# Optimization experiments

Measured on AMD Instinct MI355X. Metric: run time of the kernel, lower is better.

## Reference

```python
import jax, jax.numpy as jnp
import numpy as np

K, PS, WS, WT, NHEADS, STRIDE0_A, STRIDE0 = 7, 7, 8, 1, 1, 8, 4
SCALE = STRIDE0_A // STRIDE0  # index-upsampling factor (coarse stride 8 -> fine stride 4)


def _reflect(i, L):
    # dnls-style reflect bounds: i<0 -> -i, i>=L -> 2*(L-1)-i (single reflection suffices here)
    i = jnp.abs(i)
    return jnp.where(i >= L, 2 * (L - 1) - i, i)


def _patch_offsets(ps):
    pr = jnp.arange(ps) - ps // 2
    return jnp.stack(jnp.meshgrid(pr, pr, indexing='ij'), -1).reshape(-1, 2)  # [ps*ps, 2]


def _exact_search(vid0, vid1):
    # coarse windowed patch-product k-NN search (prod_with_heads), stride0_a query grid
    B, T, C, H, W = vid0.shape
    HD, Ch = NHEADS, C // NHEADS
    v0 = jnp.moveaxis(vid0, 2, -1)  # [B,T,H,W,C]
    v1 = jnp.moveaxis(vid1, 2, -1)
    nH, nW = H // STRIDE0_A, W // STRIDE0_A
    qt, qi, qj = [a.reshape(-1) for a in jnp.meshgrid(jnp.arange(T), jnp.arange(nH), jnp.arange(nW), indexing='ij')]
    qh, qw = qi * STRIDE0_A, qj * STRIDE0_A
    Q = qt.shape[0]
    st = 2 * WT + 1  # temporal window, shifted to stay in [0,T)
    t0 = jnp.clip(qt - WT, 0, T - st)
    offs = jnp.arange(WS) - WS // 2  # spatial window offsets, stride1=1
    ct = jnp.broadcast_to((t0[:, None] + jnp.arange(st))[:, :, None, None], (Q, st, WS, WS)).reshape(Q, -1)
    ch = jnp.broadcast_to((qh[:, None] + offs)[:, None, :, None], (Q, st, WS, WS)).reshape(Q, -1)
    cw = jnp.broadcast_to((qw[:, None] + offs)[:, None, None, :], (Q, st, WS, WS)).reshape(Q, -1)
    S = st * WS * WS
    poffs = _patch_offsets(PS)

    def body(acc, off):  # accumulate patch inner products one patch-pixel at a time (memory-light)
        dr, dc = off[0], off[1]
        p0 = v0[:, qt, _reflect(qh + dr, H), _reflect(qw + dc, W)]   # [B,Q,C]
        p1 = v1[:, ct, _reflect(ch + dr, H), _reflect(cw + dc, W)]   # [B,Q,S,C]
        d = jnp.einsum('bqnc,bqsnc->bnqs', p0.reshape(B, Q, HD, Ch), p1.reshape(B, Q, S, HD, Ch))
        return acc + d, None

    dists, _ = jax.lax.scan(jax.checkpoint(body), jnp.zeros((B, HD, Q, S), v0.dtype), poffs)
    vals, idx = jax.lax.top_k(dists, K)  # product search -> largest first
    qsel = jnp.arange(Q)[None, None, :, None]
    inds = jnp.stack([ct[qsel, idx], ch[qsel, idx], cw[qsel, idx]], -1)  # [B,HD,Q,K,3]
    return vals, inds


def _upsample_inds(inds_a, T, H, W):
    # interpolate_inds: replicate coarse inds to the fine stride0 grid, shifted by the
    # fine-query offset relative to its parent coarse query; anchor self at slot 0.
    nH, nW = H // STRIDE0_A, W // STRIDE0_A
    nHf, nWf = H // STRIDE0, W // STRIDE0
    ft, fi, fj = [a.reshape(-1) for a in jnp.meshgrid(jnp.arange(T), jnp.arange(nHf), jnp.arange(nWf), indexing='ij')]
    fh, fw = fi * STRIDE0, fj * STRIDE0
    ci = jnp.clip(fi // SCALE, 0, nH - 1)
    cj = jnp.clip(fj // SCALE, 0, nW - 1)
    qlin = ft * nH * nW + ci * nW + cj
    base = inds_a[:, :, qlin]  # [B,HD,Qf,K,3]
    dh = (fh - ci * STRIDE0_A)[None, None, :, None]
    dw = (fw - cj * STRIDE0_A)[None, None, :, None]
    it = base[..., 0]
    ih = _reflect(base[..., 1] + dh, H)
    iw = _reflect(base[..., 2] + dw, W)
    it = it.at[..., 0].set(ft[None, None, :])  # anchor_self=True
    ih = ih.at[..., 0].set(fh[None, None, :])
    iw = iw.at[..., 0].set(fw[None, None, :])
    return (ft, fh, fw), (it, ih, iw)


def _refine_dists(vid0, vid1, fq, cand):
    # prod_refine with ws_r=1: evaluate the patch product exactly at the given inds
    B, T, C, H, W = vid0.shape
    HD, Ch = NHEADS, C // NHEADS
    ft, fh, fw = fq
    it, ih, iw = cand
    Qf, k = it.shape[2], it.shape[3]
    v0 = jnp.moveaxis(vid0, 2, -1)                                # [B,T,H,W,C]
    v1h = jnp.moveaxis(vid1, 2, -1).reshape(B, T, H, W, HD, Ch)
    bidx = jnp.arange(B)[:, None, None, None]
    hidx = jnp.arange(HD)[None, :, None, None]
    poffs = _patch_offsets(PS)

    def body(acc, off):
        dr, dc = off[0], off[1]
        p0 = v0[:, ft, _reflect(fh + dr, H), _reflect(fw + dc, W)]              # [B,Qf,C]
        p1 = v1h[bidx, it, _reflect(ih + dr, H), _reflect(iw + dc, W), hidx]    # [B,HD,Qf,k,Ch]
        d = jnp.einsum('bqnc,bnqkc->bnqk', p0.reshape(B, Qf, HD, Ch), p1)
        return acc + d, None

    dists, _ = jax.lax.scan(jax.checkpoint(body), jnp.zeros((B, HD, Qf, k), v0.dtype), poffs)
    return dists


def setup_inputs() -> dict:
    key = jax.random.key(0)
    k0, k1 = jax.random.split(key)
    B, T, C, H, W = 1, 3, 64, 192, 192
    vid0 = jax.random.normal(k0, (B, T, C, H, W), dtype=jnp.float32)
    vid1 = jax.random.normal(k1, (B, T, C, H, W), dtype=jnp.float32)
    flows = jnp.zeros((B, T, 2, H, W), dtype=jnp.float32)  # accepted but unused (fflow/bflow=None)
    return {"vid0": vid0, "vid1": vid1, "flows": flows}


def reference(vid0, vid1, flows):
    B, T, C, H, W = vid0.shape
    dists_a, inds_a = _exact_search(vid0, vid1)            # coarse stride0_a search
    fq, cand = _upsample_inds(inds_a, T, H, W)             # interpolate inds to stride0 grid
    dists_f = _refine_dists(vid0, vid1, fq, cand)          # refine (fill) dists at fine inds
    inds_f = jnp.stack(cand, -1)                           # [B,HD,Qf,K,3]
    return dists_f, inds_f
```

## Files before the change

kernel.cpp:

```cpp
#include <hip/hip_runtime.h>
#include <math.h>

#define TT   3
#define CC   64
#define HH   192
#define WW   192
#define HWW  (HH*WW)
#define NHC  24
#define NWC  24
#define QC   1728
#define SC   192
#define NPIX 49
#define KK   7
#define NHF  48
#define NWF  48
#define QF   6912

__device__ __forceinline__ int reflect(int i, int L) {
  i = i < 0 ? -i : i;
  return (i >= L) ? (2 * (L - 1) - i) : i;
}

__global__ void transpose_tchw_thwc(const float* __restrict__ in0,
                                    const float* __restrict__ in1,
                                    float* __restrict__ out0,
                                    float* __restrict__ out1) {
  const float* in = blockIdx.y ? in1 : in0;
  float* out = blockIdx.y ? out1 : out0;
  int b = blockIdx.x;
  int x0 = (b % 3) * 64;
  int ty = b / 3;
  int t = ty / HH, y = ty % HH;

  __shared__ float tile[64][65];
  int lx = threadIdx.x & 63;
  int lc = threadIdx.x >> 6;

  const float* src = in + (size_t)t * CC * HWW + (size_t)y * WW + x0;
#pragma unroll
  for (int i = 0; i < 16; ++i) {
    int c = lc + i * 4;
    tile[c][lx] = src[(size_t)c * HWW + lx];
  }
  __syncthreads();
  float* dst = out + ((size_t)(t * HH + y) * WW + x0) * CC;
#pragma unroll
  for (int i = 0; i < 16; ++i) {
    int x = lc + i * 4;
    dst[(size_t)x * CC + lx] = tile[lx][x];
  }
}

__global__ __launch_bounds__(256, 3) void coarse_fma_kernel(
    const float* __restrict__ v0, const float* __restrict__ v1,
    float* __restrict__ dists) {
  int bid = blockIdx.x;
  int q = (bid & 7) * (QC / 8) + (bid >> 3);
  int qt = q / (NHC * NWC);
  int r = q % (NHC * NWC);
  int qh = (r / NWC) * 8;
  int qw = (r % NWC) * 8;

  __shared__ float4 region4[8 * 196];
  __shared__ float4 qbuf4[16 * 49];
  __shared__ float  wbuf[64 * 49];

  int tid = threadIdx.x;
  int s = tid & 63;
  int w = tid >> 6;
  int oi = s >> 3, oj = s & 7;

  int pxb[13];
#pragma unroll
  for (int i = 0; i < 13; ++i) {
    int p = w + 4 * i;
    if (p > 48) p = 48;
    pxb[i] = ((oi + p / 7) * 14 + (oj + p % 7)) * 16;
  }

  {
    const float* b0 = v0 + (size_t)qt * HWW * CC;
    for (int idx = tid; idx < 896; idx += 256) {
      int p = (idx & 7) | ((idx >> 7) << 3);
      int c4 = (idx >> 3) & 15;
      if (p < 49) {
        int ry = reflect(qh + p / 7 - 3, HH);
        int rx = reflect(qw + p % 7 - 3, WW);
        qbuf4[c4 * 49 + p] = *reinterpret_cast<const float4*>(
            b0 + ((size_t)ry * WW + rx) * CC + c4 * 4);
      }
    }
  }

  for (int ct = 0; ct < 3; ++ct) {
    const float* b1 = v1 + (size_t)ct * HWW * CC;
    float acc[13];
#pragma unroll
    for (int i = 0; i < 13; ++i) acc[i] = 0.f;

#pragma unroll
    for (int h = 0; h < 2; ++h) {
      __syncthreads();
      for (int idx = tid; idx < 1600; idx += 256) {
        int px = (idx & 7) | ((idx >> 6) << 3);
        int c4h = (idx >> 3) & 7;
        if (px < 196) {
          int ry = reflect(qh - 7 + px / 14, HH);
          int rx = reflect(qw - 7 + px % 14, WW);
          region4[c4h * 196 + px] = *reinterpret_cast<const float4*>(
              b1 + ((size_t)ry * WW + rx) * CC + (h * 8 + c4h) * 4);
        }
      }
      __syncthreads();

#pragma unroll
      for (int i = 0; i < 13; ++i) {
        if (i < 12 || w == 0) {
          int p = w + 4 * i;
          const char* rbase = reinterpret_cast<const char*>(region4) + pxb[i];
#pragma unroll
          for (int c4h = 0; c4h < 8; ++c4h) {
            float4 a = qbuf4[(h * 8 + c4h) * 49 + p];
            float4 b = *reinterpret_cast<const float4*>(rbase + c4h * 3136);
            acc[i] = fmaf(a.x, b.x, acc[i]);
            acc[i] = fmaf(a.y, b.y, acc[i]);
            acc[i] = fmaf(a.z, b.z, acc[i]);
            acc[i] = fmaf(a.w, b.w, acc[i]);
          }
        }
      }
    }

#pragma unroll
    for (int i = 0; i < 13; ++i) {
      if (i < 12 || w == 0) wbuf[s * 49 + (w + 4 * i)] = acc[i];
    }
    __syncthreads();
    if (tid < 64) {
      float a = 0.f;
      const float* wr = wbuf + tid * 49;
      for (int p = 0; p < NPIX; ++p)
        a = __fadd_rn(a, wr[p]);
      dists[(size_t)q * SC + ct * 64 + tid] = a;
    }
  }
}

__global__ __launch_bounds__(256) void topk_kernel(
    const float* __restrict__ dists, int* __restrict__ topk) {
  int q = blockIdx.x * 4 + (threadIdx.x >> 6);
  if (q >= QC) return;
  int lane = threadIdx.x & 63;
  const float* d = dists + (size_t)q * SC;
  float v[3] = {d[lane], d[lane + 64], d[lane + 128]};
  int tk = 0;
#pragma unroll
  for (int k = 0; k < KK; ++k) {
    float bv = -INFINITY;
    int bi = 0x7fffffff;
#pragma unroll
    for (int j = 0; j < 3; ++j) {
      if (!((tk >> j) & 1) && v[j] > bv) { bv = v[j]; bi = lane + j * 64; }
    }
#pragma unroll
    for (int off = 32; off > 0; off >>= 1) {
      float ov = __shfl_xor(bv, off, 64);
      int oi = __shfl_xor(bi, off, 64);
      if (ov > bv || (ov == bv && oi < bi)) { bv = ov; bi = oi; }
    }
    if ((bi & 63) == lane) tk |= 1 << (bi >> 6);
    if (lane == 0) topk[q * KK + k] = bi;
  }
}

__global__ __launch_bounds__(448, 7) void refine_kernel(
    const float* __restrict__ v0, const float* __restrict__ v1,
    const int* __restrict__ topk, float* __restrict__ out) {
  int bid = blockIdx.x;
  int f = (bid & 7) * (QF / 8) + (bid >> 3);
  int ft = f / (NHF * NWF);
  int r = f % (NHF * NWF);
  int fi = r / NWF, fj = r % NWF;
  int fh = fi * 4, fw = fj * 4;
  int ci = fi >> 1, cj = fj >> 1;
  int dh = (fi & 1) * 4, dw = (fj & 1) * 4;
  int qlin = ft * (NHC * NWC) + ci * NWC + cj;

  int tid = threadIdx.x;
  int lane = tid & 63;
  int k = tid >> 6;

  __shared__ float qs[NPIX * CC];

  {
    const float* b0 = v0 + (size_t)ft * HWW * CC;
#pragma unroll
    for (int i = 0; i < 7; ++i) {
      int idx = tid + i * 448;
      int p = idx >> 6, c = idx & 63;
      int ry = reflect(fh + p / 7 - 3, HH);
      int rx = reflect(fw + p % 7 - 3, WW);
      qs[idx] = b0[((size_t)ry * WW + rx) * CC + c];
    }
  }
  __syncthreads();

  int it, ih, iw;
  if (k == 0) {
    it = ft; ih = fh; iw = fw;
  } else {
    int s = topk[qlin * KK + k];
    int ti = s >> 6;
    int oi = (s >> 3) & 7, oj = s & 7;
    it = ti;
    ih = reflect(ci * 8 + oi - 4 + dh, HH);
    iw = reflect(cj * 8 + oj - 4 + dw, WW);
  }

  const float* b1 = v1 + (size_t)it * HWW * CC;
  float acc = 0.f;
#pragma unroll
  for (int pr = 0; pr < 7; ++pr) {
    int ry = reflect(ih + pr - 3, HH);
    const float* rowp = b1 + (size_t)ry * WW * CC + lane;
    float vals[7];
#pragma unroll
    for (int pc = 0; pc < 7; ++pc) {
      int rx = reflect(iw + pc - 3, WW);
      vals[pc] = rowp[(size_t)rx * CC];
    }
#pragma unroll
    for (int pc = 0; pc < 7; ++pc)
      acc = fmaf(qs[(pr * 7 + pc) * CC + lane], vals[pc], acc);
  }
#pragma unroll
  for (int off = 32; off > 0; off >>= 1)
    acc += __shfl_xor(acc, off, 64);
  if (lane == 0) {
    float* dout = out;
    float* iout = out + (size_t)QF * KK;
    dout[(size_t)f * KK + k] = acc;
    float* ip = iout + ((size_t)f * KK + k) * 3;
    ip[0] = (float)it;
    ip[1] = (float)ih;
    ip[2] = (float)iw;
  }
}

extern "C" void kernel_launch(void* const* d_in, const int* in_sizes, int n_in,
                              void* d_out, int out_size, void* d_ws,
                              size_t ws_size, hipStream_t stream) {
  const float* vid0 = (const float*)d_in[0];
  const float* vid1 = (const float*)d_in[1];
  float* out = (float*)d_out;

  char* ws = (char*)d_ws;
  float* dists = (float*)ws;
  size_t off = (size_t)QC * SC * sizeof(float);
  int* topk = (int*)(ws + off);
  off += (size_t)QC * KK * sizeof(int);
  off = (off + 255) & ~(size_t)255;
  float* v0t = (float*)(ws + off);
  size_t vbytes = (size_t)TT * HWW * CC * sizeof(float);
  float* v1t = (float*)(ws + off + vbytes);

  transpose_tchw_thwc<<<dim3(TT * HH * (WW / 64), 2), 256, 0, stream>>>(
      vid0, vid1, v0t, v1t);
  coarse_fma_kernel<<<QC, 256, 0, stream>>>(v0t, v1t, dists);
  topk_kernel<<<(QC * 64 + 255) / 256, 256, 0, stream>>>(dists, topk);
  refine_kernel<<<QF, 448, 0, stream>>>(v0t, v1t, topk, out);
}
```

Baseline: 288.0 us.

## Prefetch coarse region into registers and register-block two search offsets per thread

```diff
diff --git a/kernel.cpp b/kernel.cpp
--- a/kernel.cpp
+++ b/kernel.cpp
@@ -51,7 +51,7 @@
   }
 }
 
-__global__ __launch_bounds__(256, 3) void coarse_fma_kernel(
+__global__ __launch_bounds__(256, 4) void coarse_fma_kernel(
     const float* __restrict__ v0, const float* __restrict__ v1,
     float* __restrict__ dists) {
   int bid = blockIdx.x;
@@ -63,19 +63,39 @@
 
   __shared__ float4 region4[8 * 196];
   __shared__ float4 qbuf4[16 * 49];
-  __shared__ float  wbuf[64 * 49];
+  float* wbuf = (float*)region4;
 
   int tid = threadIdx.x;
-  int s = tid & 63;
+  int lane = tid & 63;
   int w = tid >> 6;
-  int oi = s >> 3, oj = s & 7;
-
-  int pxb[13];
-#pragma unroll
-  for (int i = 0; i < 13; ++i) {
-    int p = w + 4 * i;
+  int ph = lane >> 5;
+  int sA = lane & 31;
+  int oiA = sA >> 3, oj = sA & 7;
+  int rres = w + 4 * ph;
+
+  int pxb[7];
+#pragma unroll
+  for (int i = 0; i < 7; ++i) {
+    int p = rres + 8 * i;
     if (p > 48) p = 48;
-    pxb[i] = ((oi + p / 7) * 14 + (oj + p % 7)) * 16;
+    pxb[i] = ((oiA + p / 7) * 14 + (oj + p % 7)) * 16;
+  }
+
+  int srow[7], sdst[7];
+#pragma unroll
+  for (int j = 0; j < 7; ++j) {
+    int idx = tid + 256 * j;
+    int px = (idx & 7) | ((idx >> 6) << 3);
+    int c4h = (idx >> 3) & 7;
+    if (idx < 1600 && px < 196) {
+      int ry = reflect(qh - 7 + px / 14, HH);
+      int rx = reflect(qw - 7 + px % 14, WW);
+      srow[j] = (ry * WW + rx) * CC + c4h * 4;
+      sdst[j] = c4h * 196 + px;
+    } else {
+      srow[j] = 0;
+      sdst[j] = -1;
+    }
   }
 
   {
@@ -92,48 +112,70 @@
     }
   }
 
+  float4 rbuf[7];
+#pragma unroll
+  for (int j = 0; j < 7; ++j)
+    if (sdst[j] >= 0)
+      rbuf[j] = *reinterpret_cast<const float4*>(v1 + srow[j]);
+
   for (int ct = 0; ct < 3; ++ct) {
-    const float* b1 = v1 + (size_t)ct * HWW * CC;
-    float acc[13];
-#pragma unroll
-    for (int i = 0; i < 13; ++i) acc[i] = 0.f;
+    float accA[7], accB[7];
+#pragma unroll
+    for (int i = 0; i < 7; ++i) { accA[i] = 0.f; accB[i] = 0.f; }
 
 #pragma unroll
     for (int h = 0; h < 2; ++h) {
       __syncthreads();
-      for (int idx = tid; idx < 1600; idx += 256) {
-        int px = (idx & 7) | ((idx >> 6) << 3);
-        int c4h = (idx >> 3) & 7;
-        if (px < 196) {
-          int ry = reflect(qh - 7 + px / 14, HH);
-          int rx = reflect(qw - 7 + px % 14, WW);
-          region4[c4h * 196 + px] = *reinterpret_cast<const float4*>(
-              b1 + ((size_t)ry * WW + rx) * CC + (h * 8 + c4h) * 4);
-        }
+#pragma unroll
+      for (int j = 0; j < 7; ++j)
+        if (sdst[j] >= 0) region4[sdst[j]] = rbuf[j];
+      if (h == 0) {
+        const float* nb = v1 + (size_t)ct * HWW * CC + 32;
+#pragma unroll
+        for (int j = 0; j < 7; ++j)
+          if (sdst[j] >= 0)
+            rbuf[j] = *reinterpret_cast<const float4*>(nb + srow[j]);
+      } else if (ct < 2) {
+        const float* nb = v1 + (size_t)(ct + 1) * HWW * CC;
+#pragma unroll
+        for (int j = 0; j < 7; ++j)
+          if (sdst[j] >= 0)
+            rbuf[j] = *reinterpret_cast<const float4*>(nb + srow[j]);
       }
       __syncthreads();
 
 #pragma unroll
-      for (int i = 0; i < 13; ++i) {
-        if (i < 12 || w == 0) {
-          int p = w + 4 * i;
-          const char* rbase = reinterpret_cast<const char*>(region4) + pxb[i];
+      for (int i = 0; i < 7; ++i) {
+        if (i < 6 || rres == 0) {
+          int p = rres + 8 * i;
+          const char* ra = reinterpret_cast<const char*>(region4) + pxb[i];
 #pragma unroll
           for (int c4h = 0; c4h < 8; ++c4h) {
             float4 a = qbuf4[(h * 8 + c4h) * 49 + p];
-            float4 b = *reinterpret_cast<const float4*>(rbase + c4h * 3136);
-            acc[i] = fmaf(a.x, b.x, acc[i]);
-            acc[i] = fmaf(a.y, b.y, acc[i]);
-            acc[i] = fmaf(a.z, b.z, acc[i]);
-            acc[i] = fmaf(a.w, b.w, acc[i]);
+            float4 bA = *reinterpret_cast<const float4*>(ra + c4h * 3136);
+            float4 bB =
+                *reinterpret_cast<const float4*>(ra + c4h * 3136 + 896);
+            accA[i] = fmaf(a.x, bA.x, accA[i]);
+            accA[i] = fmaf(a.y, bA.y, accA[i]);
+            accA[i] = fmaf(a.z, bA.z, accA[i]);
+            accA[i] = fmaf(a.w, bA.w, accA[i]);
+            accB[i] = fmaf(a.x, bB.x, accB[i]);
+            accB[i] = fmaf(a.y, bB.y, accB[i]);
+            accB[i] = fmaf(a.z, bB.z, accB[i]);
+            accB[i] = fmaf(a.w, bB.w, accB[i]);
           }
         }
       }
     }
 
-#pragma unroll
-    for (int i = 0; i < 13; ++i) {
-      if (i < 12 || w == 0) wbuf[s * 49 + (w + 4 * i)] = acc[i];
+    __syncthreads();
+#pragma unroll
+    for (int i = 0; i < 7; ++i) {
+      if (i < 6 || rres == 0) {
+        int p = rres + 8 * i;
+        wbuf[sA * 49 + p] = accA[i];
+        wbuf[(sA + 32) * 49 + p] = accB[i];
+      }
     }
     __syncthreads();
     if (tid < 64) {
```

Result: slower. 305.8 us (+6.2%).
